# Kernel optimization log

Hardware: AMD Instinct MI355X
Metric: run time of the kernel (lower is better)

The kernel has to match this reference:

```python
import jax, jax.numpy as jnp
import numpy as np


def setup_inputs() -> dict:
    key = jax.random.key(0)
    k1, k2, k3, k4 = jax.random.split(key, 4)
    B, S, IN, OUT, K = 4, 2048, 4096, 4096, 256
    x = jax.random.normal(k1, (B, S, IN), dtype=jnp.float32)
    centroids = jax.random.normal(k2, (K,), dtype=jnp.float32)
    bias = jax.random.normal(k3, (OUT,), dtype=jnp.float32)
    indices = jax.random.randint(k4, (OUT, IN), 0, K, dtype=jnp.int64)
    return {"x": x, "centroids": centroids, "bias": bias, "indices": indices}


def reference(x, centroids, bias, indices):
    # Reconstruct the weight matrix from the codebook: [out, in]
    weight = centroids[indices]
    # F.linear: y = x @ weight.T + bias
    out = jnp.einsum('bsi,oi->bso', x, weight) + bias
    return out
```

## Files before the change

kernel.cpp:

```cpp
#include <hip/hip_runtime.h>
#include <hip/hip_bf16.h>
#include <stdint.h>


typedef unsigned short u16;
typedef __attribute__((ext_vector_type(8))) short short8;
typedef __attribute__((ext_vector_type(8))) u16   u16x8;
typedef __attribute__((ext_vector_type(4))) float f32x4;
typedef __attribute__((ext_vector_type(4))) int   i32x4;

constexpr int Mdim = 8192;
constexpr int Ndim = 4096;
constexpr int Kdim = 4096;

__device__ __forceinline__ u16 f2bf(float f) {
  union { float f; uint32_t u; } v; v.f = f;
  uint32_t u = v.u;
  return (u16)((u + 0x7fffu + ((u >> 16) & 1u)) >> 16);
}

__global__ void decode_weight_kernel(const int* __restrict__ idx,
                                     const float* __restrict__ cent,
                                     u16* __restrict__ wb) {
  __shared__ u16 lut[256];
  const int t = threadIdx.x;
  if (t < 256) lut[t] = f2bf(cent[t]);
  __syncthreads();
  const size_t base = ((size_t)blockIdx.x * 256 + t) * 8;
  i32x4 i0 = *(const i32x4*)(idx + base);
  i32x4 i1 = *(const i32x4*)(idx + base + 4);
  u16x8 r;
  r[0] = lut[i0[0] & 255]; r[1] = lut[i0[1] & 255];
  r[2] = lut[i0[2] & 255]; r[3] = lut[i0[3] & 255];
  r[4] = lut[i1[0] & 255]; r[5] = lut[i1[1] & 255];
  r[6] = lut[i1[2] & 255]; r[7] = lut[i1[3] & 255];
  *(u16x8*)(wb + base) = r;
}

__global__ void cvt_x_kernel(const float* __restrict__ x, u16* __restrict__ xb) {
  const size_t base = ((size_t)blockIdx.x * 256 + threadIdx.x) * 8;
  f32x4 a = *(const f32x4*)(x + base);
  f32x4 b = *(const f32x4*)(x + base + 4);
  u16x8 r;
  r[0] = f2bf(a[0]); r[1] = f2bf(a[1]); r[2] = f2bf(a[2]); r[3] = f2bf(a[3]);
  r[4] = f2bf(b[0]); r[5] = f2bf(b[1]); r[6] = f2bf(b[2]); r[7] = f2bf(b[3]);
  *(u16x8*)(xb + base) = r;
}

__device__ __forceinline__ void async16(const u16* g, u16* l) {
  __builtin_amdgcn_global_load_lds(
      (const __attribute__((address_space(1))) void*)g,
      (__attribute__((address_space(3))) void*)l,
      16, 0, 0);
}

#define BAR()   __builtin_amdgcn_s_barrier()
#define SCB()   __builtin_amdgcn_sched_barrier(0)
#define LGKM0() do { asm volatile("s_waitcnt lgkmcnt(0)" ::: "memory"); SCB(); } while (0)
#define LGKM4() do { asm volatile("s_waitcnt lgkmcnt(4)" ::: "memory"); SCB(); } while (0)
#define VMC4()  asm volatile("s_waitcnt vmcnt(4)" ::: "memory")
#define VMC0()  asm volatile("s_waitcnt vmcnt(0)" ::: "memory")

__global__ __launch_bounds__(512, 2)
void gemm_bf16_kernel(const u16* __restrict__ A,
                      const u16* __restrict__ B,
                      const float* __restrict__ bias,
                      float* __restrict__ C) {
  __shared__ u16 AsF[32768];
  __shared__ u16 BsF[32768];

  const int t    = threadIdx.x;
  const int lane = t & 63;
  const int w    = t >> 6;
  const int wm   = w >> 2;
  const int wn   = w & 3;
  const int fr   = lane & 15;
  const int fq   = lane >> 4;
  const int cswz = (fr & 6) << 2;

  const int bid = blockIdx.x;
  const int swz = (bid & 7) * 64 + (bid >> 3);
  const int m0 = (swz >> 4) * 256;
  const int n0 = (swz & 15) * 256;

  const int c0   = w * 64 + lane;
  const int r16s = (c0 & 63) >> 2;
  const int srow = ((c0 >> 7) << 4) + r16s;
  const int scol = ((c0 >> 6) & 1) * 32 + (((c0 & 3) * 8) ^ ((r16s & 6) << 2));
  const u16* pA = A + (size_t)(m0 + srow) * Kdim + scol;
  const u16* pB = B + (size_t)(n0 + srow) * Kdim + scol;
  const int dsto = c0 * 8;

  const int aoff = wm * 8192 + fr * 32 + ((fq * 8) ^ cswz);
  const int boff = (wn >> 1) * 8192 + (wn & 1) * 4096 + fr * 32 + ((fq * 8) ^ cswz);

  f32x4 acc[8][4] = {};
  short8 bf[2][4];
  short8 afA[2][2];
  short8 afB[2][2];

  auto stageA = [&](int tk, int h) {
    const u16* s = pA + (size_t)h * (128 * Kdim) + tk * 64;
    u16* d = &AsF[((tk & 1) * 2 + h) * 8192 + dsto];
    async16(s, d);
    async16(s + (size_t)(64 * Kdim), d + 4096);
  };
  auto stageB = [&](int tk, int h) {
    const u16* s = pB + (size_t)h * (128 * Kdim) + tk * 64;
    u16* d = &BsF[((tk & 1) * 2 + h) * 8192 + dsto];
    async16(s, d);
    async16(s + (size_t)(64 * Kdim), d + 4096);
  };
  auto rdB_kk = [&](int buf, int kk) {
#pragma unroll
    for (int ni = 0; ni < 4; ++ni)
      bf[kk][ni] = *(const short8*)&BsF[buf * 16384 + boff + (ni * 2 + kk) * 512];
  };
  auto rdA_A = [&](int buf, int q) {
#pragma unroll
    for (int kk = 0; kk < 2; ++kk)
#pragma unroll
      for (int i = 0; i < 2; ++i)
        afA[kk][i] = *(const short8*)&AsF[buf * 16384 + aoff + ((q * 2 + i) * 2 + kk) * 512];
  };
  auto rdA_B = [&](int buf, int q) {
#pragma unroll
    for (int kk = 0; kk < 2; ++kk)
#pragma unroll
      for (int i = 0; i < 2; ++i)
        afB[kk][i] = *(const short8*)&AsF[buf * 16384 + aoff + ((q * 2 + i) * 2 + kk) * 512];
  };
  auto mfmaE = [&](int q) {
    __builtin_amdgcn_s_setprio(1);
#pragma unroll
    for (int kk = 0; kk < 2; ++kk)
#pragma unroll
      for (int i = 0; i < 2; ++i)
#pragma unroll
        for (int ni = 0; ni < 4; ++ni)
          acc[q * 2 + i][ni] = __builtin_amdgcn_mfma_f32_16x16x32_bf16(
              afA[kk][i], bf[kk][ni], acc[q * 2 + i][ni], 0, 0, 0);
    __builtin_amdgcn_s_setprio(0);
  };
  auto mfmaO = [&](int q) {
    __builtin_amdgcn_s_setprio(1);
#pragma unroll
    for (int kk = 0; kk < 2; ++kk)
#pragma unroll
      for (int i = 0; i < 2; ++i)
#pragma unroll
        for (int ni = 0; ni < 4; ++ni)
          acc[q * 2 + i][ni] = __builtin_amdgcn_mfma_f32_16x16x32_bf16(
              afB[kk][i], bf[kk][ni], acc[q * 2 + i][ni], 0, 0, 0);
    __builtin_amdgcn_s_setprio(0);
  };
  auto mfmaO_kk = [&](int q, int kk) {
    __builtin_amdgcn_s_setprio(1);
#pragma unroll
    for (int i = 0; i < 2; ++i)
#pragma unroll
      for (int ni = 0; ni < 4; ++ni)
        acc[q * 2 + i][ni] = __builtin_amdgcn_mfma_f32_16x16x32_bf16(
            afB[kk][i], bf[kk][ni], acc[q * 2 + i][ni], 0, 0, 0);
    __builtin_amdgcn_s_setprio(0);
  };

#define KT(TK, BUF, DOA, DOB, MODE)                                     \
  {                                                                     \
                                                                \
    rdA_B((BUF), 1);                                                    \
    if (DOA) stageA((TK) + 1, 0);                                       \
    LGKM4();                  \
    mfmaE(0);                                                           \
                                                                \
    rdA_A((BUF), 2);                                                    \
    if (DOA) stageA((TK) + 1, 1);                                       \
    if (DOB) stageB((TK) + 2, 0);                                       \
    LGKM4();                                               \
    mfmaO(1);                                                           \
                                                                \
    rdA_B((BUF), 3);                                                    \
    if (DOB) stageB((TK) + 2, 1);                                       \
    LGKM4();                                               \
    mfmaE(2);                                                           \
                      \
    if ((MODE) == 0) { VMC4(); } else if ((MODE) == 1) { VMC0(); }      \
    BAR();                         \
    LGKM0();                                         \
    mfmaO_kk(3, 0);                                                     \
    if ((MODE) < 2) rdB_kk((BUF) ^ 1, 0);                               \
    mfmaO_kk(3, 1);                                                     \
    if ((MODE) < 2) { rdB_kk((BUF) ^ 1, 1); rdA_A((BUF) ^ 1, 0); }      \
  }

  stageA(0, 0); stageA(0, 1); stageB(0, 0); stageB(0, 1);
  stageB(1, 0); stageB(1, 1);
  VMC4();
  BAR();
  rdB_kk(0, 0); rdB_kk(0, 1); rdA_A(0, 0);

  for (int t2 = 0; t2 < 31; ++t2) {
    const int k0 = 2 * t2;
    KT(k0,     0, 1, 1, 0);
    KT(k0 + 1, 1, 1, 1, 0);
  }
  KT(62, 0, 1, 0, 1);
  KT(63, 1, 0, 0, 2);

  float bv[4];
#pragma unroll
  for (int ni = 0; ni < 4; ++ni)
    bv[ni] = bias[n0 + wn * 64 + ni * 16 + fr];

#pragma unroll
  for (int mi = 0; mi < 8; ++mi) {
#pragma unroll
    for (int j = 0; j < 4; ++j) {
      const int row = m0 + wm * 128 + mi * 16 + fq * 4 + j;
      float* cp = C + (size_t)row * Ndim + n0 + wn * 64 + fr;
#pragma unroll
      for (int ni = 0; ni < 4; ++ni)
        cp[ni * 16] = acc[mi][ni][j] + bv[ni];
    }
  }
#undef KT
}

extern "C" void kernel_launch(void* const* d_in, const int* in_sizes, int n_in,
                              void* d_out, int out_size, void* d_ws, size_t ws_size,
                              hipStream_t stream) {
  const float* x    = (const float*)d_in[0];
  const float* cent = (const float*)d_in[1];
  const float* bias = (const float*)d_in[2];
  const int*   idx  = (const int*)d_in[3];
  float* out = (float*)d_out;

  u16* wb = (u16*)d_ws;
  u16* xb = (u16*)((char*)d_ws + (size_t)Ndim * Kdim * sizeof(u16));

  decode_weight_kernel<<<(Ndim * Kdim) / (256 * 8), 256, 0, stream>>>(idx, cent, wb);
  cvt_x_kernel<<<((size_t)Mdim * Kdim) / (256 * 8), 256, 0, stream>>>(x, xb);

  gemm_bf16_kernel<<<dim3(512), 512, 0, stream>>>(xb, wb, bias, out);
}
```

Measured before the change: 282.8 us.

## Shrink GEMM tile to 128x128 with 256-thread blocks and XCD-aware mapping

After: 321.6 us. +13.7%, slower.

```diff
diff --git a/kernel.cpp b/kernel.cpp
--- a/kernel.cpp
+++ b/kernel.cpp
@@ -57,89 +57,86 @@
 #define BAR()   __builtin_amdgcn_s_barrier()
 #define SCB()   __builtin_amdgcn_sched_barrier(0)
 #define LGKM0() do { asm volatile("s_waitcnt lgkmcnt(0)" ::: "memory"); SCB(); } while (0)
-#define LGKM4() do { asm volatile("s_waitcnt lgkmcnt(4)" ::: "memory"); SCB(); } while (0)
+#define LGKM2() do { asm volatile("s_waitcnt lgkmcnt(2)" ::: "memory"); SCB(); } while (0)
 #define VMC4()  asm volatile("s_waitcnt vmcnt(4)" ::: "memory")
 #define VMC0()  asm volatile("s_waitcnt vmcnt(0)" ::: "memory")
 
-__global__ __launch_bounds__(512, 2)
+__global__ __launch_bounds__(256, 2)
 void gemm_bf16_kernel(const u16* __restrict__ A,
                       const u16* __restrict__ B,
                       const float* __restrict__ bias,
                       float* __restrict__ C) {
-  __shared__ u16 AsF[32768];
-  __shared__ u16 BsF[32768];
+  __shared__ u16 AsF[16384];
+  __shared__ u16 BsF[16384];
 
   const int t    = threadIdx.x;
   const int lane = t & 63;
   const int w    = t >> 6;
-  const int wm   = w >> 2;
-  const int wn   = w & 3;
+  const int wm   = w >> 1;
+  const int wn   = w & 1;
   const int fr   = lane & 15;
   const int fq   = lane >> 4;
   const int cswz = (fr & 6) << 2;
 
-  const int bid = blockIdx.x;
-  const int swz = (bid & 7) * 64 + (bid >> 3);
-  const int m0 = (swz >> 4) * 256;
-  const int n0 = (swz & 15) * 256;
-
-  const int c0   = w * 64 + lane;
-  const int r16s = (c0 & 63) >> 2;
-  const int srow = ((c0 >> 7) << 4) + r16s;
-  const int scol = ((c0 >> 6) & 1) * 32 + (((c0 & 3) * 8) ^ ((r16s & 6) << 2));
-  const u16* pA = A + (size_t)(m0 + srow) * Kdim + scol;
-  const u16* pB = B + (size_t)(n0 + srow) * Kdim + scol;
-  const int dsto = c0 * 8;
-
-  const int aoff = wm * 8192 + fr * 32 + ((fq * 8) ^ cswz);
-  const int boff = (wn >> 1) * 8192 + (wn & 1) * 4096 + fr * 32 + ((fq * 8) ^ cswz);
-
-  f32x4 acc[8][4] = {};
+  const int bid   = blockIdx.x;
+  const int xcd   = bid & 7;
+  const int wi    = (bid >> 3) & 31;
+  const int round = bid >> 8;
+  const int mt = xcd * 8 + (wi >> 2);
+  const int nt = round * 4 + (wi & 3);
+  const int m0 = mt * 128;
+  const int n0 = nt * 128;
+
+  int srcOff[4];
+#pragma unroll
+  for (int l = 0; l < 4; ++l) {
+    const int c    = t + l * 256;
+    const int r16s = (c & 63) >> 2;
+    const int srow = ((c >> 7) << 4) + r16s;
+    const int scol = ((c >> 6) & 1) * 32 + (((c & 3) * 8) ^ ((r16s & 6) << 2));
+    srcOff[l] = srow * Kdim + scol;
+  }
+  const int dsto = t * 8;
+  const u16* pA = A + (size_t)m0 * Kdim;
+  const u16* pB = B + (size_t)n0 * Kdim;
+
+  const int aBase = fr * 32 + ((fq * 8) ^ cswz);
+  const int bBase = fr * 32 + ((fq * 8) ^ cswz);
+
+  f32x4 acc[4][4] = {};
   short8 bf[2][4];
-  short8 afA[2][2];
-  short8 afB[2][2];
-
-  auto stageA = [&](int tk, int h) {
-    const u16* s = pA + (size_t)h * (128 * Kdim) + tk * 64;
-    u16* d = &AsF[((tk & 1) * 2 + h) * 8192 + dsto];
-    async16(s, d);
-    async16(s + (size_t)(64 * Kdim), d + 4096);
-  };
-  auto stageB = [&](int tk, int h) {
-    const u16* s = pB + (size_t)h * (128 * Kdim) + tk * 64;
-    u16* d = &BsF[((tk & 1) * 2 + h) * 8192 + dsto];
-    async16(s, d);
-    async16(s + (size_t)(64 * Kdim), d + 4096);
+  short8 afE[2];
+  short8 afO[2];
+
+  auto stA = [&](int tk, int l) {
+    async16(pA + srcOff[l] + tk * 64, &AsF[((tk & 1) << 13) + dsto + l * 2048]);
+  };
+  auto stB = [&](int tk, int l) {
+    async16(pB + srcOff[l] + tk * 64, &BsF[((tk & 1) << 13) + dsto + l * 2048]);
   };
   auto rdB_kk = [&](int buf, int kk) {
 #pragma unroll
     for (int ni = 0; ni < 4; ++ni)
-      bf[kk][ni] = *(const short8*)&BsF[buf * 16384 + boff + (ni * 2 + kk) * 512];
-  };
-  auto rdA_A = [&](int buf, int q) {
-#pragma unroll
-    for (int kk = 0; kk < 2; ++kk)
-#pragma unroll
-      for (int i = 0; i < 2; ++i)
-        afA[kk][i] = *(const short8*)&AsF[buf * 16384 + aoff + ((q * 2 + i) * 2 + kk) * 512];
-  };
-  auto rdA_B = [&](int buf, int q) {
-#pragma unroll
-    for (int kk = 0; kk < 2; ++kk)
-#pragma unroll
-      for (int i = 0; i < 2; ++i)
-        afB[kk][i] = *(const short8*)&AsF[buf * 16384 + aoff + ((q * 2 + i) * 2 + kk) * 512];
+      bf[kk][ni] = *(const short8*)&BsF[(buf << 13) + bBase + (wn * 4 + ni) * 1024 + kk * 512];
+  };
+  auto rdA_E = [&](int buf, int mi) {
+#pragma unroll
+    for (int kk = 0; kk < 2; ++kk)
+      afE[kk] = *(const short8*)&AsF[(buf << 13) + aBase + (wm * 4 + mi) * 1024 + kk * 512];
+  };
+  auto rdA_O = [&](int buf, int mi) {
+#pragma unroll
+    for (int kk = 0; kk < 2; ++kk)
+      afO[kk] = *(const short8*)&AsF[(buf << 13) + aBase + (wm * 4 + mi) * 1024 + kk * 512];
   };
   auto mfmaE = [&](int q) {
     __builtin_amdgcn_s_setprio(1);
 #pragma unroll
     for (int kk = 0; kk < 2; ++kk)
 #pragma unroll
-      for (int i = 0; i < 2; ++i)
-#pragma unroll
-        for (int ni = 0; ni < 4; ++ni)
-          acc[q * 2 + i][ni] = __builtin_amdgcn_mfma_f32_16x16x32_bf16(
-              afA[kk][i], bf[kk][ni], acc[q * 2 + i][ni], 0, 0, 0);
+      for (int ni = 0; ni < 4; ++ni)
+        acc[q][ni] = __builtin_amdgcn_mfma_f32_16x16x32_bf16(
+            afE[kk], bf[kk][ni], acc[q][ni], 0, 0, 0);
     __builtin_amdgcn_s_setprio(0);
   };
   auto mfmaO = [&](int q) {
@@ -147,41 +144,37 @@
 #pragma unroll
     for (int kk = 0; kk < 2; ++kk)
 #pragma unroll
-      for (int i = 0; i < 2; ++i)
-#pragma unroll
-        for (int ni = 0; ni < 4; ++ni)
-          acc[q * 2 + i][ni] = __builtin_amdgcn_mfma_f32_16x16x32_bf16(
-              afB[kk][i], bf[kk][ni], acc[q * 2 + i][ni], 0, 0, 0);
+      for (int ni = 0; ni < 4; ++ni)
+        acc[q][ni] = __builtin_amdgcn_mfma_f32_16x16x32_bf16(
+            afO[kk], bf[kk][ni], acc[q][ni], 0, 0, 0);
     __builtin_amdgcn_s_setprio(0);
   };
   auto mfmaO_kk = [&](int q, int kk) {
     __builtin_amdgcn_s_setprio(1);
 #pragma unroll
-    for (int i = 0; i < 2; ++i)
-#pragma unroll
-      for (int ni = 0; ni < 4; ++ni)
-        acc[q * 2 + i][ni] = __builtin_amdgcn_mfma_f32_16x16x32_bf16(
-            afB[kk][i], bf[kk][ni], acc[q * 2 + i][ni], 0, 0, 0);
+    for (int ni = 0; ni < 4; ++ni)
+      acc[q][ni] = __builtin_amdgcn_mfma_f32_16x16x32_bf16(
+          afO[kk], bf[kk][ni], acc[q][ni], 0, 0, 0);
     __builtin_amdgcn_s_setprio(0);
   };
 
 #define KT(TK, BUF, DOA, DOB, MODE)                                     \
   {                                                                     \
                                                                 \
-    rdA_B((BUF), 1);                                                    \
-    if (DOA) stageA((TK) + 1, 0);                                       \
-    LGKM4();                  \
+    rdA_O((BUF), 1);                                                    \
+    if (DOA) { stA((TK) + 1, 0); stA((TK) + 1, 1); }                    \
+    LGKM2();                        \
     mfmaE(0);                                                           \
                                                                 \
-    rdA_A((BUF), 2);                                                    \
-    if (DOA) stageA((TK) + 1, 1);                                       \
-    if (DOB) stageB((TK) + 2, 0);                                       \
-    LGKM4();                                               \
+    rdA_E((BUF), 2);                                                    \
+    if (DOA) { stA((TK) + 1, 2); stA((TK) + 1, 3); }                    \
+    if (DOB) { stB((TK) + 2, 0); stB((TK) + 2, 1); }                    \
+    LGKM2();                                               \
     mfmaO(1);                                                           \
                                                                 \
-    rdA_B((BUF), 3);                                                    \
-    if (DOB) stageB((TK) + 2, 1);                                       \
-    LGKM4();                                               \
+    rdA_O((BUF), 3);                                                    \
+    if (DOB) { stB((TK) + 2, 2); stB((TK) + 2, 3); }                    \
+    LGKM2();                                               \
     mfmaE(2);                                                           \
                       \
     if ((MODE) == 0) { VMC4(); } else if ((MODE) == 1) { VMC0(); }      \
@@ -190,19 +183,22 @@
     mfmaO_kk(3, 0);                                                     \
     if ((MODE) < 2) rdB_kk((BUF) ^ 1, 0);                               \
     mfmaO_kk(3, 1);                                                     \
-    if ((MODE) < 2) { rdB_kk((BUF) ^ 1, 1); rdA_A((BUF) ^ 1, 0); }      \
-  }
-
-  stageA(0, 0); stageA(0, 1); stageB(0, 0); stageB(0, 1);
-  stageB(1, 0); stageB(1, 1);
+    if ((MODE) < 2) { rdB_kk((BUF) ^ 1, 1); rdA_E((BUF) ^ 1, 0); }      \
+  }
+
+#pragma unroll
+  for (int l = 0; l < 4; ++l) stA(0, l);
+#pragma unroll
+  for (int l = 0; l < 4; ++l) stB(0, l);
+#pragma unroll
+  for (int l = 0; l < 4; ++l) stB(1, l);
   VMC4();
   BAR();
-  rdB_kk(0, 0); rdB_kk(0, 1); rdA_A(0, 0);
+  rdB_kk(0, 0); rdB_kk(0, 1); rdA_E(0, 0);
 
   for (int t2 = 0; t2 < 31; ++t2) {
-    const int k0 = 2 * t2;
-    KT(k0,     0, 1, 1, 0);
-    KT(k0 + 1, 1, 1, 1, 0);
+    KT(2 * t2,     0, 1, 1, 0);
+    KT(2 * t2 + 1, 1, 1, 1, 0);
   }
   KT(62, 0, 1, 0, 1);
   KT(63, 1, 0, 0, 2);
@@ -213,10 +209,10 @@
     bv[ni] = bias[n0 + wn * 64 + ni * 16 + fr];
 
 #pragma unroll
-  for (int mi = 0; mi < 8; ++mi) {
+  for (int mi = 0; mi < 4; ++mi) {
 #pragma unroll
     for (int j = 0; j < 4; ++j) {
-      const int row = m0 + wm * 128 + mi * 16 + fq * 4 + j;
+      const int row = m0 + wm * 64 + mi * 16 + fq * 4 + j;
       float* cp = C + (size_t)row * Ndim + n0 + wn * 64 + fr;
 #pragma unroll
       for (int ni = 0; ni < 4; ++ni)
@@ -241,5 +237,5 @@
   decode_weight_kernel<<<(Ndim * Kdim) / (256 * 8), 256, 0, stream>>>(idx, cent, wb);
   cvt_x_kernel<<<((size_t)Mdim * Kdim) / (256 * 8), 256, 0, stream>>>(x, xb);
 
-  gemm_bf16_kernel<<<dim3(512), 512, 0, stream>>>(xb, wb, bias, out);
-}
+  gemm_bf16_kernel<<<dim3(2048), 256, 0, stream>>>(xb, wb, bias, out);
+}
```

## Load B fragments directly from global into registers, dropping B LDS staging

Applied to the files above, without the earlier changes.

New measurement: 342.4 us, median of 2. 1.21x slower.

```diff
diff --git a/kernel.cpp b/kernel.cpp
--- a/kernel.cpp
+++ b/kernel.cpp
@@ -58,8 +58,11 @@
 #define SCB()   __builtin_amdgcn_sched_barrier(0)
 #define LGKM0() do { asm volatile("s_waitcnt lgkmcnt(0)" ::: "memory"); SCB(); } while (0)
 #define LGKM4() do { asm volatile("s_waitcnt lgkmcnt(4)" ::: "memory"); SCB(); } while (0)
+#define VMC8()  asm volatile("s_waitcnt vmcnt(8)" ::: "memory")
 #define VMC4()  asm volatile("s_waitcnt vmcnt(4)" ::: "memory")
-#define VMC0()  asm volatile("s_waitcnt vmcnt(0)" ::: "memory")
+#define VMC4S() do { asm volatile("s_waitcnt vmcnt(4)" ::: "memory"); SCB(); } while (0)
+#define VMC2S() do { asm volatile("s_waitcnt vmcnt(2)" ::: "memory"); SCB(); } while (0)
+#define VMC0S() do { asm volatile("s_waitcnt vmcnt(0)" ::: "memory"); SCB(); } while (0)
 
 __global__ __launch_bounds__(512, 2)
 void gemm_bf16_kernel(const u16* __restrict__ A,
@@ -67,7 +70,6 @@
                       const float* __restrict__ bias,
                       float* __restrict__ C) {
   __shared__ u16 AsF[32768];
-  __shared__ u16 BsF[32768];
 
   const int t    = threadIdx.x;
   const int lane = t & 63;
@@ -87,35 +89,24 @@
   const int r16s = (c0 & 63) >> 2;
   const int srow = ((c0 >> 7) << 4) + r16s;
   const int scol = ((c0 >> 6) & 1) * 32 + (((c0 & 3) * 8) ^ ((r16s & 6) << 2));
-  const u16* pA = A + (size_t)(m0 + srow) * Kdim + scol;
-  const u16* pB = B + (size_t)(n0 + srow) * Kdim + scol;
   const int dsto = c0 * 8;
+  const u16* pa0 = A + (size_t)(m0 + srow) * Kdim + scol;
+  const u16* pa1 = pa0 + (size_t)64  * Kdim;
+  const u16* pa2 = pa0 + (size_t)128 * Kdim;
+  const u16* pa3 = pa0 + (size_t)192 * Kdim;
+
+  const u16* bp0 = B + (size_t)(n0 + wn * 64 +  0 + fr) * Kdim + fq * 8;
+  const u16* bp1 = B + (size_t)(n0 + wn * 64 + 16 + fr) * Kdim + fq * 8;
+  const u16* bp2 = B + (size_t)(n0 + wn * 64 + 32 + fr) * Kdim + fq * 8;
+  const u16* bp3 = B + (size_t)(n0 + wn * 64 + 48 + fr) * Kdim + fq * 8;
 
   const int aoff = wm * 8192 + fr * 32 + ((fq * 8) ^ cswz);
-  const int boff = (wn >> 1) * 8192 + (wn & 1) * 4096 + fr * 32 + ((fq * 8) ^ cswz);
 
   f32x4 acc[8][4] = {};
   short8 bf[2][4];
   short8 afA[2][2];
   short8 afB[2][2];
 
-  auto stageA = [&](int tk, int h) {
-    const u16* s = pA + (size_t)h * (128 * Kdim) + tk * 64;
-    u16* d = &AsF[((tk & 1) * 2 + h) * 8192 + dsto];
-    async16(s, d);
-    async16(s + (size_t)(64 * Kdim), d + 4096);
-  };
-  auto stageB = [&](int tk, int h) {
-    const u16* s = pB + (size_t)h * (128 * Kdim) + tk * 64;
-    u16* d = &BsF[((tk & 1) * 2 + h) * 8192 + dsto];
-    async16(s, d);
-    async16(s + (size_t)(64 * Kdim), d + 4096);
-  };
-  auto rdB_kk = [&](int buf, int kk) {
-#pragma unroll
-    for (int ni = 0; ni < 4; ++ni)
-      bf[kk][ni] = *(const short8*)&BsF[buf * 16384 + boff + (ni * 2 + kk) * 512];
-  };
   auto rdA_A = [&](int buf, int q) {
 #pragma unroll
     for (int kk = 0; kk < 2; ++kk)
@@ -130,28 +121,26 @@
       for (int i = 0; i < 2; ++i)
         afB[kk][i] = *(const short8*)&AsF[buf * 16384 + aoff + ((q * 2 + i) * 2 + kk) * 512];
   };
-  auto mfmaE = [&](int q) {
+  auto bfload0 = [&]() {
+    asm volatile("global_load_dwordx4 %0, %1, off" : "=v"(bf[0][0]) : "v"(bp0) : "memory");
+    asm volatile("global_load_dwordx4 %0, %1, off" : "=v"(bf[0][1]) : "v"(bp1) : "memory");
+    asm volatile("global_load_dwordx4 %0, %1, off" : "=v"(bf[0][2]) : "v"(bp2) : "memory");
+    asm volatile("global_load_dwordx4 %0, %1, off" : "=v"(bf[0][3]) : "v"(bp3) : "memory");
+  };
+  auto bfload1 = [&]() {
+    asm volatile("global_load_dwordx4 %0, %1, off offset:64" : "=v"(bf[1][0]) : "v"(bp0) : "memory");
+    asm volatile("global_load_dwordx4 %0, %1, off offset:64" : "=v"(bf[1][1]) : "v"(bp1) : "memory");
+    asm volatile("global_load_dwordx4 %0, %1, off offset:64" : "=v"(bf[1][2]) : "v"(bp2) : "memory");
+    asm volatile("global_load_dwordx4 %0, %1, off offset:64" : "=v"(bf[1][3]) : "v"(bp3) : "memory");
+  };
+  auto mfmaE_kk = [&](int q, int kk) {
     __builtin_amdgcn_s_setprio(1);
 #pragma unroll
-    for (int kk = 0; kk < 2; ++kk)
-#pragma unroll
-      for (int i = 0; i < 2; ++i)
-#pragma unroll
-        for (int ni = 0; ni < 4; ++ni)
-          acc[q * 2 + i][ni] = __builtin_amdgcn_mfma_f32_16x16x32_bf16(
-              afA[kk][i], bf[kk][ni], acc[q * 2 + i][ni], 0, 0, 0);
-    __builtin_amdgcn_s_setprio(0);
-  };
-  auto mfmaO = [&](int q) {
-    __builtin_amdgcn_s_setprio(1);
-#pragma unroll
-    for (int kk = 0; kk < 2; ++kk)
-#pragma unroll
-      for (int i = 0; i < 2; ++i)
-#pragma unroll
-        for (int ni = 0; ni < 4; ++ni)
-          acc[q * 2 + i][ni] = __builtin_amdgcn_mfma_f32_16x16x32_bf16(
-              afB[kk][i], bf[kk][ni], acc[q * 2 + i][ni], 0, 0, 0);
+    for (int i = 0; i < 2; ++i)
+#pragma unroll
+      for (int ni = 0; ni < 4; ++ni)
+        acc[q * 2 + i][ni] = __builtin_amdgcn_mfma_f32_16x16x32_bf16(
+            afA[kk][i], bf[kk][ni], acc[q * 2 + i][ni], 0, 0, 0);
     __builtin_amdgcn_s_setprio(0);
   };
   auto mfmaO_kk = [&](int q, int kk) {
@@ -165,47 +154,74 @@
     __builtin_amdgcn_s_setprio(0);
   };
 
-#define KT(TK, BUF, DOA, DOB, MODE)                                     \
-  {                                                                     \
-                                                                \
-    rdA_B((BUF), 1);                                                    \
-    if (DOA) stageA((TK) + 1, 0);                                       \
-    LGKM4();                  \
-    mfmaE(0);                                                           \
-                                                                \
-    rdA_A((BUF), 2);                                                    \
-    if (DOA) stageA((TK) + 1, 1);                                       \
-    if (DOB) stageB((TK) + 2, 0);                                       \
-    LGKM4();                                               \
-    mfmaO(1);                                                           \
-                                                                \
-    rdA_B((BUF), 3);                                                    \
-    if (DOB) stageB((TK) + 2, 1);                                       \
-    LGKM4();                                               \
-    mfmaE(2);                                                           \
-                      \
-    if ((MODE) == 0) { VMC4(); } else if ((MODE) == 1) { VMC0(); }      \
-    BAR();                         \
-    LGKM0();                                         \
-    mfmaO_kk(3, 0);                                                     \
-    if ((MODE) < 2) rdB_kk((BUF) ^ 1, 0);                               \
-    mfmaO_kk(3, 1);                                                     \
-    if ((MODE) < 2) { rdB_kk((BUF) ^ 1, 1); rdA_A((BUF) ^ 1, 0); }      \
-  }
-
-  stageA(0, 0); stageA(0, 1); stageB(0, 0); stageB(0, 1);
-  stageB(1, 0); stageB(1, 1);
-  VMC4();
+#define KT(BUF)                                                          \
+  {                                                                      \
+                                                                 \
+    rdA_B((BUF), 1);                                                     \
+    LGKM4();                              \
+    VMC4S();                                            \
+    mfmaE_kk(0, 0);                                                      \
+    async16(pa0, &AsF[((BUF ^ 1) * 2 + 0) * 8192 + dsto]);               \
+    async16(pa1, &AsF[((BUF ^ 1) * 2 + 0) * 8192 + 4096 + dsto]);        \
+    VMC2S();                           \
+    mfmaE_kk(0, 1);                                                      \
+                                                                 \
+    rdA_A((BUF), 2);                                                     \
+    async16(pa2, &AsF[((BUF ^ 1) * 2 + 1) * 8192 + dsto]);               \
+    async16(pa3, &AsF[((BUF ^ 1) * 2 + 1) * 8192 + 4096 + dsto]);        \
+    LGKM4();                                                \
+    mfmaO_kk(1, 0); mfmaO_kk(1, 1);                                      \
+                                                                 \
+    rdA_B((BUF), 3);                                                     \
+    LGKM4();                                                \
+    mfmaE_kk(2, 0); mfmaE_kk(2, 1);                                      \
+                                                                 \
+    LGKM0();                                                \
+    mfmaO_kk(3, 0);                                                      \
+    bfload0();                  \
+    VMC4();                     \
+    BAR();                                                               \
+    rdA_A((BUF) ^ 1, 0);                   \
+    mfmaO_kk(3, 1);                                                      \
+    bfload1();                  \
+    pa0 += 64; pa1 += 64; pa2 += 64; pa3 += 64;                          \
+    bp0 += 64; bp1 += 64; bp2 += 64; bp3 += 64;                          \
+  }
+
+  async16(pa0, &AsF[0 * 8192 + dsto]);
+  async16(pa1, &AsF[0 * 8192 + 4096 + dsto]);
+  async16(pa2, &AsF[1 * 8192 + dsto]);
+  async16(pa3, &AsF[1 * 8192 + 4096 + dsto]);
+  bfload0();
+  bfload1();
+  pa0 += 64; pa1 += 64; pa2 += 64; pa3 += 64;
+  bp0 += 64; bp1 += 64; bp2 += 64; bp3 += 64;
+  VMC8();
   BAR();
-  rdB_kk(0, 0); rdB_kk(0, 1); rdA_A(0, 0);
+  rdA_A(0, 0);
 
   for (int t2 = 0; t2 < 31; ++t2) {
-    const int k0 = 2 * t2;
-    KT(k0,     0, 1, 1, 0);
-    KT(k0 + 1, 1, 1, 1, 0);
-  }
-  KT(62, 0, 1, 0, 1);
-  KT(63, 1, 0, 0, 2);
+    KT(0);
+    KT(1);
+  }
+  KT(0);
+
+  {
+    rdA_B(1, 1);
+    LGKM4();
+    VMC4S();
+    mfmaE_kk(0, 0);
+    VMC0S();
+    mfmaE_kk(0, 1);
+    rdA_A(1, 2);
+    LGKM4();
+    mfmaO_kk(1, 0); mfmaO_kk(1, 1);
+    rdA_B(1, 3);
+    LGKM4();
+    mfmaE_kk(2, 0); mfmaE_kk(2, 1);
+    LGKM0();
+    mfmaO_kk(3, 0); mfmaO_kk(3, 1);
+  }
 
   float bv[4];
 #pragma unroll
```
